# Kernel tuning notes

Measured on AMD Instinct MI355X. Metric: run time of the kernel, lower is better.

## Reference

```python
import jax, jax.numpy as jnp
import numpy as np

B, L, D = 32, 512, 768


def setup_inputs() -> dict:
    key = jax.random.key(0)
    k1, k2 = jax.random.split(key)
    sent_we = jax.random.normal(k1, (B, L, D), dtype=jnp.float32)
    # two entity positions per example, values in [0, L)
    idxs = jax.random.randint(k2, (B, 2), 0, L)
    return {"sent_we": sent_we, "idxs": idxs}


def reference(sent_we, idxs):
    # fuzzy_type='concat', context_size=1, is_use_norm=False, is_use_scale=False
    idxs = idxs.astype(jnp.int32)
    # one_hot(idxs, L) @ sent_we  ==  direct gather of entity vectors -> [B, 2, D]
    entity_we = jnp.take_along_axis(sent_we, idxs[:, :, None], axis=1)
    # attention scores of each entity vs every token: [B, 2, L]
    att = jnp.einsum('bkd,bld->bkl', entity_we, sent_we)
    # repeat att along feature dim and multiply == broadcast per-token scalar;
    # concat branch: [sent_we * att_e1, sent_we * att_e2] -> [B, L, 2D]
    new_we = jnp.concatenate(
        [sent_we * att[:, 0, :, None], sent_we * att[:, 1, :, None]], axis=-1)
    return new_we
```

## Files before the change

kernel.cpp:

```cpp
#include <hip/hip_runtime.h>


constexpr int B = 32;
constexpr int L = 512;
constexpr int D = 768;
constexpr int THREADS = 192;

__global__ __launch_bounds__(THREADS)
void efca_kernel(const float* __restrict__ sent,
                 const int* __restrict__ idxs,
                 float* __restrict__ out) {
    const int bl = blockIdx.x;
    const int b  = bl >> 9;
    const int l  = bl & (L - 1);
    const int t  = threadIdx.x;

    const float4* __restrict__ row =
        reinterpret_cast<const float4*>(sent + (size_t)(b * L + l) * D);
    const int i0 = idxs[b * 2 + 0];
    const int i1 = idxs[b * 2 + 1];
    const float4* __restrict__ e0 =
        reinterpret_cast<const float4*>(sent + (size_t)(b * L + i0) * D);
    const float4* __restrict__ e1 =
        reinterpret_cast<const float4*>(sent + (size_t)(b * L + i1) * D);

    const float4 r  = row[t];
    const float4 a  = e0[t];
    const float4 c  = e1[t];

    float p0 = r.x * a.x + r.y * a.y + r.z * a.z + r.w * a.w;
    float p1 = r.x * c.x + r.y * c.y + r.z * c.z + r.w * c.w;

    #pragma unroll
    for (int off = 32; off > 0; off >>= 1) {
        p0 += __shfl_down(p0, off, 64);
        p1 += __shfl_down(p1, off, 64);
    }

    __shared__ float s0[3], s1[3];
    __shared__ float fa0, fa1;
    const int wave = t >> 6;
    const int lane = t & 63;
    if (lane == 0) { s0[wave] = p0; s1[wave] = p1; }
    __syncthreads();
    if (t == 0) {
        fa0 = s0[0] + s0[1] + s0[2];
        fa1 = s1[0] + s1[1] + s1[2];
    }
    __syncthreads();
    const float a0 = fa0;
    const float a1 = fa1;

    float4* __restrict__ o =
        reinterpret_cast<float4*>(out + (size_t)(b * L + l) * (2 * D));
    o[t]           = make_float4(r.x * a0, r.y * a0, r.z * a0, r.w * a0);
    o[t + THREADS] = make_float4(r.x * a1, r.y * a1, r.z * a1, r.w * a1);
}

extern "C" void kernel_launch(void* const* d_in, const int* in_sizes, int n_in,
                              void* d_out, int out_size, void* d_ws, size_t ws_size,
                              hipStream_t stream) {
    const float* sent = (const float*)d_in[0];
    const int*   idxs = (const int*)d_in[1];
    float*       out  = (float*)d_out;

    dim3 grid(B * L);
    dim3 block(THREADS);
    efca_kernel<<<grid, block, 0, stream>>>(sent, idxs, out);
}
```

Baseline: 139.1 us.

## Assign one wave per row, drop LDS reduction, use nontemporal loads/stores

Each 64-lane wave now processes a whole row (three float4 per lane), so the dot products finish with a wave-level xor shuffle and no shared memory or __syncthreads. Blocks hold four waves, each on its own row. Row loads and output stores use nontemporal hints so streaming data does not evict the reused entity rows from cache. Per-thread register use goes up and the grid has fewer blocks.

Result: no change. 139.6 us, median of 2 (+0.4%).

```diff
diff --git a/kernel.cpp b/kernel.cpp
--- a/kernel.cpp
+++ b/kernel.cpp
@@ -4,57 +4,57 @@
 constexpr int B = 32;
 constexpr int L = 512;
 constexpr int D = 768;
-constexpr int THREADS = 192;
+constexpr int WAVES = 4;
+constexpr int THREADS = 64 * WAVES;
+constexpr int NBLK = (B * L) / WAVES;
+
+typedef float f4 __attribute__((ext_vector_type(4)));
+
+__device__ __forceinline__ float dot4(f4 a, f4 b) {
+    f4 p = a * b;
+    return (p.x + p.y) + (p.z + p.w);
+}
 
 __global__ __launch_bounds__(THREADS)
 void efca_kernel(const float* __restrict__ sent,
                  const int* __restrict__ idxs,
                  float* __restrict__ out) {
-    const int bl = blockIdx.x;
-    const int b  = bl >> 9;
-    const int l  = bl & (L - 1);
-    const int t  = threadIdx.x;
+    const int wave = threadIdx.x >> 6;
+    const int lane = threadIdx.x & 63;
+    const int bl   = blockIdx.x * WAVES + wave;
+    const int b    = bl >> 9;
 
-    const float4* __restrict__ row =
-        reinterpret_cast<const float4*>(sent + (size_t)(b * L + l) * D);
+    const f4* __restrict__ row =
+        reinterpret_cast<const f4*>(sent + (size_t)bl * D);
     const int i0 = idxs[b * 2 + 0];
     const int i1 = idxs[b * 2 + 1];
-    const float4* __restrict__ e0 =
-        reinterpret_cast<const float4*>(sent + (size_t)(b * L + i0) * D);
-    const float4* __restrict__ e1 =
-        reinterpret_cast<const float4*>(sent + (size_t)(b * L + i1) * D);
+    const f4* __restrict__ e0 =
+        reinterpret_cast<const f4*>(sent + (size_t)(b * L + i0) * D);
+    const f4* __restrict__ e1 =
+        reinterpret_cast<const f4*>(sent + (size_t)(b * L + i1) * D);
 
-    const float4 r  = row[t];
-    const float4 a  = e0[t];
-    const float4 c  = e1[t];
+    const f4 r0 = __builtin_nontemporal_load(row + lane);
+    const f4 r1 = __builtin_nontemporal_load(row + lane + 64);
+    const f4 r2 = __builtin_nontemporal_load(row + lane + 128);
+    const f4 a0 = e0[lane], a1 = e0[lane + 64], a2 = e0[lane + 128];
+    const f4 c0 = e1[lane], c1 = e1[lane + 64], c2 = e1[lane + 128];
 
-    float p0 = r.x * a.x + r.y * a.y + r.z * a.z + r.w * a.w;
-    float p1 = r.x * c.x + r.y * c.y + r.z * c.z + r.w * c.w;
+    float p0 = dot4(r0, a0) + dot4(r1, a1) + dot4(r2, a2);
+    float p1 = dot4(r0, c0) + dot4(r1, c1) + dot4(r2, c2);
 
     #pragma unroll
     for (int off = 32; off > 0; off >>= 1) {
-        p0 += __shfl_down(p0, off, 64);
-        p1 += __shfl_down(p1, off, 64);
+        p0 += __shfl_xor(p0, off, 64);
+        p1 += __shfl_xor(p1, off, 64);
     }
 
-    __shared__ float s0[3], s1[3];
-    __shared__ float fa0, fa1;
-    const int wave = t >> 6;
-    const int lane = t & 63;
-    if (lane == 0) { s0[wave] = p0; s1[wave] = p1; }
-    __syncthreads();
-    if (t == 0) {
-        fa0 = s0[0] + s0[1] + s0[2];
-        fa1 = s1[0] + s1[1] + s1[2];
-    }
-    __syncthreads();
-    const float a0 = fa0;
-    const float a1 = fa1;
-
-    float4* __restrict__ o =
-        reinterpret_cast<float4*>(out + (size_t)(b * L + l) * (2 * D));
-    o[t]           = make_float4(r.x * a0, r.y * a0, r.z * a0, r.w * a0);
-    o[t + THREADS] = make_float4(r.x * a1, r.y * a1, r.z * a1, r.w * a1);
+    f4* __restrict__ o = reinterpret_cast<f4*>(out + (size_t)bl * (2 * D));
+    __builtin_nontemporal_store(r0 * p0, o + lane);
+    __builtin_nontemporal_store(r1 * p0, o + lane + 64);
+    __builtin_nontemporal_store(r2 * p0, o + lane + 128);
+    __builtin_nontemporal_store(r0 * p1, o + lane + 192);
+    __builtin_nontemporal_store(r1 * p1, o + lane + 256);
+    __builtin_nontemporal_store(r2 * p1, o + lane + 320);
 }
 
 extern "C" void kernel_launch(void* const* d_in, const int* in_sizes, int n_in,
@@ -64,7 +64,5 @@
     const int*   idxs = (const int*)d_in[1];
     float*       out  = (float*)d_out;
 
-    dim3 grid(B * L);
-    dim3 block(THREADS);
-    efca_kernel<<<grid, block, 0, stream>>>(sent, idxs, out);
+    efca_kernel<<<dim3(NBLK), dim3(THREADS), 0, stream>>>(sent, idxs, out);
 }
```
